# Optimization experiments

Measured on AMD Instinct MI355X. Metric: run time of the kernel, lower is better.

Reference implementation:

```python
import jax, jax.numpy as jnp
import numpy as np

DEG_U = 3
DEG_V = 3
EPS = 1e-6


def uniform_knot_vectors(n_cp, degree, n_surf, n_fac):
    # first `degree` zeros, linspace(0,1) over the middle, last `degree` ones
    interior = jnp.linspace(0.0, 1.0, n_cp + degree + 1 - 2 * degree, dtype=jnp.float32)
    kv = jnp.concatenate([jnp.zeros(degree, jnp.float32), interior, jnp.ones(degree, jnp.float32)])
    return jnp.broadcast_to(kv, (n_surf, n_fac, kv.shape[0]))


def find_spans_uniform(u, n_cp, degree):
    # uniform clamped knot vector: n_unique = n_cp - degree + 1 distinct knots
    n_unique = n_cp - degree + 1
    return jnp.floor(u * (n_unique - 1)).astype(jnp.int32) + degree


def basis_funs_and_derivs(u, span, knots, p, n=1):
    """NURBS Book A2.3, vectorized over [S,F,P]. Returns ders[k][j] arrays."""
    def kn(off):
        return jnp.take_along_axis(knots, span + off, axis=2)

    left = [None] * (p + 1)
    right = [None] * (p + 1)
    ndu = [[None] * (p + 1) for _ in range(p + 1)]
    ndu[0][0] = jnp.ones_like(u)
    for j in range(1, p + 1):
        left[j] = u - kn(1 - j)
        right[j] = kn(j) - u
        saved = jnp.zeros_like(u)
        for r in range(j):
            ndu[j][r] = right[r + 1] + left[j - r]
            temp = ndu[r][j - 1] / ndu[j][r]
            ndu[r][j] = saved + right[r + 1] * temp
            saved = left[j - r] * temp
        ndu[j][j] = saved

    ders = [[None] * (p + 1) for _ in range(n + 1)]
    for j in range(p + 1):
        ders[0][j] = ndu[j][p]
    for r in range(p + 1):
        s1, s2 = 0, 1
        a = [[jnp.zeros_like(u) for _ in range(p + 1)] for _ in range(2)]
        a[0][0] = jnp.ones_like(u)
        for k in range(1, n + 1):
            d = jnp.zeros_like(u)
            rk, pk = r - k, p - k
            if r >= k:
                a[s2][0] = a[s1][0] / ndu[pk + 1][rk]
                d = a[s2][0] * ndu[rk][pk]
            j1 = 1 if rk >= -1 else -rk
            j2 = k - 1 if r - 1 <= pk else p - r
            for jj in range(j1, j2 + 1):
                a[s2][jj] = (a[s1][jj] - a[s1][jj - 1]) / ndu[pk + 1][rk + jj]
                d = d + a[s2][jj] * ndu[rk + jj][pk]
            if r <= pk:
                a[s2][k] = -a[s1][k - 1] / ndu[pk + 1][r]
                d = d + a[s2][k] * ndu[r][pk]
            ders[k][r] = d
            s1, s2 = s2, s1
    fac = float(p)
    for k in range(1, n + 1):
        for j in range(p + 1):
            ders[k][j] = ders[k][j] * fac
        fac *= p - k
    return ders


def setup_inputs() -> dict:
    key = jax.random.key(0)
    k1, k2 = jax.random.split(key)
    S, F, P = 8, 4, 200000
    Ncu, Ncv = 32, 32
    evaluation_points = jax.random.uniform(k1, (S, F, P, 2), dtype=jnp.float32) * (1.0 - EPS)
    control_points = jax.random.normal(k2, (S, F, Ncu, Ncv, 3), dtype=jnp.float32)
    return {"evaluation_points": evaluation_points, "control_points": control_points}


def reference(evaluation_points, control_points):
    S, F, Ncu, Ncv, _ = control_points.shape
    u = evaluation_points[..., 0]  # [S,F,P]
    v = evaluation_points[..., 1]
    knots_u = uniform_knot_vectors(Ncu, DEG_U, S, F)
    knots_v = uniform_knot_vectors(Ncv, DEG_V, S, F)
    span_u = find_spans_uniform(u, Ncu, DEG_U)
    span_v = find_spans_uniform(v, Ncv, DEG_V)
    du_basis = basis_funs_and_derivs(u, span_u, knots_u, DEG_U, 1)
    dv_basis = basis_funs_and_derivs(v, span_v, knots_v, DEG_V, 1)

    bs = jnp.arange(S)[:, None, None]
    bf = jnp.arange(F)[None, :, None]
    pt = 0.0
    d_u = 0.0
    d_v = 0.0
    for i in range(DEG_U + 1):
        iu = span_u - DEG_U + i  # [S,F,P]
        Nu0 = du_basis[0][i][..., None]
        Nu1 = du_basis[1][i][..., None]
        for j in range(DEG_V + 1):
            iv = span_v - DEG_V + j
            cpij = control_points[bs, bf, iu, iv]  # [S,F,P,3]
            Nv0 = dv_basis[0][j][..., None]
            Nv1 = dv_basis[1][j][..., None]
            pt = pt + Nu0 * Nv0 * cpij
            d_u = d_u + Nu1 * Nv0 * cpij
            d_v = d_v + Nu0 * Nv1 * cpij
    normals = jnp.cross(d_u, d_v)
    normals = normals / (jnp.linalg.norm(normals, axis=-1, keepdims=True) + 1e-12)
    return pt, normals
```

## Files before the change

kernel.cpp:

```cpp
#include <hip/hip_runtime.h>


#define NCP 32
#define KMAX 29

__device__ __forceinline__ float rcp29(int d) {
    return (d == 1) ? 29.0f : ((d == 2) ? 14.5f : (29.0f / 3.0f));
}

__device__ __forceinline__ void basis3(float u, int a, float B0[4], float B1[4]) {
    const float s = 1.0f / 29.0f;
    float km2 = (float)max(a - 2, 0) * s;
    float km1 = (float)max(a - 1, 0) * s;
    float k00 = (float)a * s;
    float kp1 = (float)(a + 1) * s;
    float kp2 = (float)min(a + 2, KMAX) * s;
    float kp3 = (float)min(a + 3, KMAX) * s;
    float l1 = u - k00;
    float l2 = u - km1;
    float l3 = u - km2;
    float r1 = kp1 - u;
    float r2 = kp2 - u;
    float r3 = kp3 - u;
    float q20 = rcp29(min(a + 1, 2));
    float q21 = rcp29(min(KMAX - a, 2));
    float q30 = rcp29(min(a + 1, 3));
    float q31 = rcp29(min(min(a + 2, 30 - a), 3));
    float q32 = rcp29(min(KMAX - a, 3));
    float n01 = r1 * 29.0f;
    float n11 = l1 * 29.0f;
    float t = n01 * q20;
    float n02 = r1 * t;
    float sv = l2 * t;
    t = n11 * q21;
    float n12 = fmaf(r2, t, sv);
    float n22 = l1 * t;
    float t0 = n02 * q30;
    B0[0] = r1 * t0;
    sv = l3 * t0;
    float t1 = n12 * q31;
    B0[1] = fmaf(r2, t1, sv);
    sv = l2 * t1;
    float t2 = n22 * q32;
    B0[2] = fmaf(r3, t2, sv);
    B0[3] = l1 * t2;
    B1[0] = -3.0f * t0;
    B1[1] = 3.0f * (t0 - t1);
    B1[2] = 3.0f * (t1 - t2);
    B1[3] = 3.0f * t2;
}

__global__ __launch_bounds__(256) void nurbs_eval_kernel(
    const float2* __restrict__ ev,
    const float*  __restrict__ cp,
    float* __restrict__ out_pt,
    float* __restrict__ out_nrm,
    int P)
{
    __shared__ float sx[NCP * NCP];
    __shared__ float sy[NCP * NCP];
    __shared__ float sz[NCP * NCP];

    const int sf = blockIdx.y;
    const float* g = cp + (size_t)sf * (NCP * NCP * 3);
    for (int i = threadIdx.x; i < NCP * NCP; i += blockDim.x) {
        float c0 = g[3 * i + 0];
        float c1 = g[3 * i + 1];
        float c2 = g[3 * i + 2];
        sx[i] = c0; sy[i] = c1; sz[i] = c2;
    }
    __syncthreads();

    const int p = blockIdx.x * blockDim.x + threadIdx.x;
    if (p >= P) return;
    const int t = sf * P + p;

    float2 uv = ev[t];
    float u = uv.x, v = uv.y;
    int au = (int)floorf(u * 29.0f);
    int av = (int)floorf(v * 29.0f);
    au = min(max(au, 0), 28);
    av = min(max(av, 0), 28);

    float B0u[4], B1u[4], B0v[4], B1v[4];
    basis3(u, au, B0u, B1u);
    basis3(v, av, B0v, B1v);

    float px = 0.f, py = 0.f, pz = 0.f;
    float ux = 0.f, uy = 0.f, uz = 0.f;
    float vx = 0.f, vy = 0.f, vz = 0.f;
    const int base = au * NCP + av;
#pragma unroll
    for (int i = 0; i < 4; ++i) {
        const int rb = base + i * NCP;
        float rpx = 0.f, rpy = 0.f, rpz = 0.f;
        float rvx = 0.f, rvy = 0.f, rvz = 0.f;
#pragma unroll
        for (int j = 0; j < 4; ++j) {
            float cx = sx[rb + j];
            float cy = sy[rb + j];
            float cz = sz[rb + j];
            float b0 = B0v[j], b1 = B1v[j];
            rpx = fmaf(b0, cx, rpx); rpy = fmaf(b0, cy, rpy); rpz = fmaf(b0, cz, rpz);
            rvx = fmaf(b1, cx, rvx); rvy = fmaf(b1, cy, rvy); rvz = fmaf(b1, cz, rvz);
        }
        float bu0 = B0u[i], bu1 = B1u[i];
        px = fmaf(bu0, rpx, px); py = fmaf(bu0, rpy, py); pz = fmaf(bu0, rpz, pz);
        ux = fmaf(bu1, rpx, ux); uy = fmaf(bu1, rpy, uy); uz = fmaf(bu1, rpz, uz);
        vx = fmaf(bu0, rvx, vx); vy = fmaf(bu0, rvy, vy); vz = fmaf(bu0, rvz, vz);
    }

    float nx = uy * vz - uz * vy;
    float ny = uz * vx - ux * vz;
    float nz = ux * vy - uy * vx;
    float len = sqrtf(nx * nx + ny * ny + nz * nz);
    float inv = 1.0f / (len + 1e-12f);
    nx *= inv; ny *= inv; nz *= inv;

    const int o = t * 3;
    out_pt[o + 0] = px;
    out_pt[o + 1] = py;
    out_pt[o + 2] = pz;
    out_nrm[o + 0] = nx;
    out_nrm[o + 1] = ny;
    out_nrm[o + 2] = nz;
}

extern "C" void kernel_launch(void* const* d_in, const int* in_sizes, int n_in,
                              void* d_out, int out_size, void* d_ws, size_t ws_size,
                              hipStream_t stream) {
    (void)n_in; (void)d_ws; (void)ws_size;
    const int SF = in_sizes[1] / (NCP * NCP * 3);
    const int P  = in_sizes[0] / (SF * 2);
    const int N  = SF * P;
    (void)out_size;

    const float2* ev = (const float2*)d_in[0];
    const float*  cp = (const float*)d_in[1];
    float* out_pt  = (float*)d_out;
    float* out_nrm = (float*)d_out + (size_t)N * 3;

    dim3 block(256);
    dim3 grid((P + 255) / 256, SF);
    nurbs_eval_kernel<<<grid, block, 0, stream>>>(ev, cp, out_pt, out_nrm, P);
}
```

Before: 231.4 us.

## Stage control-point 4-wide windows in LDS and enlarge blocks to 1024 threads

Control points are now staged in shared memory as pre-packed windows of four consecutive points stored as three float4s, so each row of the 4x4 stencil takes three vector LDS reads instead of twelve scalar ones. Blocks grow from 256 to 1024 threads, which spreads each block's staging cost over more points. The span clamp is simplified and sqrt/reciprocal use the fast hardware builtins. Shared memory rises to about 48KB per block, which limits how many blocks fit per CU, and the fast rcp/sqrt may change low-order bits.

```diff
diff --git a/kernel.cpp b/kernel.cpp
--- a/kernel.cpp
+++ b/kernel.cpp
@@ -16,12 +16,8 @@
     float kp1 = (float)(a + 1) * s;
     float kp2 = (float)min(a + 2, KMAX) * s;
     float kp3 = (float)min(a + 3, KMAX) * s;
-    float l1 = u - k00;
-    float l2 = u - km1;
-    float l3 = u - km2;
-    float r1 = kp1 - u;
-    float r2 = kp2 - u;
-    float r3 = kp3 - u;
+    float l1 = u - k00, l2 = u - km1, l3 = u - km2;
+    float r1 = kp1 - u, r2 = kp2 - u, r3 = kp3 - u;
     float q20 = rcp29(min(a + 1, 2));
     float q21 = rcp29(min(KMAX - a, 2));
     float q30 = rcp29(min(a + 1, 3));
@@ -50,24 +46,29 @@
     B1[3] = 3.0f * t2;
 }
 
-__global__ __launch_bounds__(256) void nurbs_eval_kernel(
+__global__ __launch_bounds__(1024, 8) void nurbs_eval_kernel(
     const float2* __restrict__ ev,
     const float*  __restrict__ cp,
     float* __restrict__ out_pt,
     float* __restrict__ out_nrm,
     int P)
 {
-    __shared__ float sx[NCP * NCP];
-    __shared__ float sy[NCP * NCP];
-    __shared__ float sz[NCP * NCP];
+    __shared__ float4 win[NCP * NCP * 3];
 
     const int sf = blockIdx.y;
     const float* g = cp + (size_t)sf * (NCP * NCP * 3);
-    for (int i = threadIdx.x; i < NCP * NCP; i += blockDim.x) {
-        float c0 = g[3 * i + 0];
-        float c1 = g[3 * i + 1];
-        float c2 = g[3 * i + 2];
-        sx[i] = c0; sy[i] = c1; sz[i] = c2;
+    for (int idx = threadIdx.x; idx < NCP * 29; idx += blockDim.x) {
+        int row = idx / 29;
+        int c   = idx - row * 29;
+        const float* r = g + (row * NCP + c) * 3;
+        float x0 = r[0], y0 = r[1],  z0 = r[2];
+        float x1 = r[3], y1 = r[4],  z1 = r[5];
+        float x2 = r[6], y2 = r[7],  z2 = r[8];
+        float x3 = r[9], y3 = r[10], z3 = r[11];
+        int w = (row * NCP + c) * 3;
+        win[w + 0] = make_float4(x0, y0, z0, x1);
+        win[w + 1] = make_float4(y1, z1, x2, y2);
+        win[w + 2] = make_float4(z2, x3, y3, z3);
     }
     __syncthreads();
 
@@ -76,45 +77,46 @@
     const int t = sf * P + p;
 
     float2 uv = ev[t];
-    float u = uv.x, v = uv.y;
-    int au = (int)floorf(u * 29.0f);
-    int av = (int)floorf(v * 29.0f);
-    au = min(max(au, 0), 28);
-    av = min(max(av, 0), 28);
+    int au = min((int)(uv.x * 29.0f), 28);
+    int av = min((int)(uv.y * 29.0f), 28);
 
     float B0u[4], B1u[4], B0v[4], B1v[4];
-    basis3(u, au, B0u, B1u);
-    basis3(v, av, B0v, B1v);
+    basis3(uv.x, au, B0u, B1u);
+    basis3(uv.y, av, B0v, B1v);
+    const float bv0 = B0v[0], bv1 = B0v[1], bv2 = B0v[2], bv3 = B0v[3];
+    const float dv0 = B1v[0], dv1 = B1v[1], dv2 = B1v[2], dv3 = B1v[3];
 
     float px = 0.f, py = 0.f, pz = 0.f;
     float ux = 0.f, uy = 0.f, uz = 0.f;
     float vx = 0.f, vy = 0.f, vz = 0.f;
-    const int base = au * NCP + av;
+    const int base = (au * NCP + av) * 3;
 #pragma unroll
     for (int i = 0; i < 4; ++i) {
-        const int rb = base + i * NCP;
-        float rpx = 0.f, rpy = 0.f, rpz = 0.f;
-        float rvx = 0.f, rvy = 0.f, rvz = 0.f;
-#pragma unroll
-        for (int j = 0; j < 4; ++j) {
-            float cx = sx[rb + j];
-            float cy = sy[rb + j];
-            float cz = sz[rb + j];
-            float b0 = B0v[j], b1 = B1v[j];
-            rpx = fmaf(b0, cx, rpx); rpy = fmaf(b0, cy, rpy); rpz = fmaf(b0, cz, rpz);
-            rvx = fmaf(b1, cx, rvx); rvy = fmaf(b1, cy, rvy); rvz = fmaf(b1, cz, rvz);
-        }
-        float bu0 = B0u[i], bu1 = B1u[i];
-        px = fmaf(bu0, rpx, px); py = fmaf(bu0, rpy, py); pz = fmaf(bu0, rpz, pz);
-        ux = fmaf(bu1, rpx, ux); uy = fmaf(bu1, rpy, uy); uz = fmaf(bu1, rpz, uz);
-        vx = fmaf(bu0, rvx, vx); vy = fmaf(bu0, rvy, vy); vz = fmaf(bu0, rvz, vz);
+        const float4 q0 = win[base + i * (NCP * 3) + 0];
+        const float4 q1 = win[base + i * (NCP * 3) + 1];
+        const float4 q2 = win[base + i * (NCP * 3) + 2];
+        const float cx0 = q0.x, cy0 = q0.y, cz0 = q0.z;
+        const float cx1 = q0.w, cy1 = q1.x, cz1 = q1.y;
+        const float cx2 = q1.z, cy2 = q1.w, cz2 = q2.x;
+        const float cx3 = q2.y, cy3 = q2.z, cz3 = q2.w;
+        float rpx = fmaf(bv3, cx3, fmaf(bv2, cx2, fmaf(bv1, cx1, bv0 * cx0)));
+        float rpy = fmaf(bv3, cy3, fmaf(bv2, cy2, fmaf(bv1, cy1, bv0 * cy0)));
+        float rpz = fmaf(bv3, cz3, fmaf(bv2, cz2, fmaf(bv1, cz1, bv0 * cz0)));
+        float rvx = fmaf(dv3, cx3, fmaf(dv2, cx2, fmaf(dv1, cx1, dv0 * cx0)));
+        float rvy = fmaf(dv3, cy3, fmaf(dv2, cy2, fmaf(dv1, cy1, dv0 * cy0)));
+        float rvz = fmaf(dv3, cz3, fmaf(dv2, cz2, fmaf(dv1, cz1, dv0 * cz0)));
+        const float bu = B0u[i], du = B1u[i];
+        px = fmaf(bu, rpx, px); py = fmaf(bu, rpy, py); pz = fmaf(bu, rpz, pz);
+        ux = fmaf(du, rpx, ux); uy = fmaf(du, rpy, uy); uz = fmaf(du, rpz, uz);
+        vx = fmaf(bu, rvx, vx); vy = fmaf(bu, rvy, vy); vz = fmaf(bu, rvz, vz);
     }
 
     float nx = uy * vz - uz * vy;
     float ny = uz * vx - ux * vz;
     float nz = ux * vy - uy * vx;
-    float len = sqrtf(nx * nx + ny * ny + nz * nz);
-    float inv = 1.0f / (len + 1e-12f);
+    float d   = fmaf(nx, nx, fmaf(ny, ny, nz * nz));
+    float len = __builtin_amdgcn_sqrtf(d);
+    float inv = __builtin_amdgcn_rcpf(len + 1e-12f);
     nx *= inv; ny *= inv; nz *= inv;
 
     const int o = t * 3;
@@ -129,18 +131,17 @@
 extern "C" void kernel_launch(void* const* d_in, const int* in_sizes, int n_in,
                               void* d_out, int out_size, void* d_ws, size_t ws_size,
                               hipStream_t stream) {
-    (void)n_in; (void)d_ws; (void)ws_size;
+    (void)n_in; (void)d_ws; (void)ws_size; (void)out_size;
     const int SF = in_sizes[1] / (NCP * NCP * 3);
     const int P  = in_sizes[0] / (SF * 2);
     const int N  = SF * P;
-    (void)out_size;
 
     const float2* ev = (const float2*)d_in[0];
     const float*  cp = (const float*)d_in[1];
     float* out_pt  = (float*)d_out;
     float* out_nrm = (float*)d_out + (size_t)N * 3;
 
-    dim3 block(256);
-    dim3 grid((P + 255) / 256, SF);
+    dim3 block(1024);
+    dim3 grid((P + 1023) / 1024, SF);
     nurbs_eval_kernel<<<grid, block, 0, stream>>>(ev, cp, out_pt, out_nrm, P);
 }
```

Result: faster. 209.6 us (-9.4%).
